# Kernel tuning notes

Hardware: AMD Instinct MI355X
Metric: run time of the kernel (lower is better)

Reference implementation:

```python
import jax, jax.numpy as jnp
import numpy as np

N, E = 50000, 800000
IN, HID, OUT = 128, 128, 64
H, ED = 4, 3
D = HID // H  # per-head dim = 32


def _w(key, shape):
    fan_in = shape[-1]
    return jax.random.normal(key, shape, dtype=jnp.float32) / np.sqrt(fan_in)


def setup_inputs() -> dict:
    key = jax.random.key(0)
    ks = jax.random.split(key, 32)
    inp = {
        "x": jax.random.normal(ks[0], (N, IN), dtype=jnp.float32),
        "edge_index": jax.random.randint(ks[1], (2, E), 0, N, dtype=jnp.int32),
        "edge_attr": jax.random.normal(ks[2], (E, ED), dtype=jnp.float32),
        # layer 1 TransformerConv (bias=False)
        "Wq1": _w(ks[3], (HID, IN)), "Wk1": _w(ks[4], (HID, IN)),
        "Wv1": _w(ks[5], (HID, IN)), "We1": _w(ks[6], (HID, ED)),
        "Ws1": _w(ks[7], (HID, IN)),
        # layer 1 MLP [HID,HID,HID]
        "M1a": _w(ks[8], (HID, HID)), "b1a": jnp.zeros((HID,), jnp.float32),
        "M1b": _w(ks[9], (HID, HID)), "b1b": jnp.zeros((HID,), jnp.float32),
        # layer 2 TransformerConv
        "Wq2": _w(ks[10], (HID, HID)), "Wk2": _w(ks[11], (HID, HID)),
        "Wv2": _w(ks[12], (HID, HID)), "We2": _w(ks[13], (HID, ED)),
        "Ws2": _w(ks[14], (HID, HID)),
        # layer 2 MLP
        "M2a": _w(ks[15], (HID, HID)), "b2a": jnp.zeros((HID,), jnp.float32),
        "M2b": _w(ks[16], (HID, HID)), "b2b": jnp.zeros((HID,), jnp.float32),
        # final MLP [HID,HID,OUT], plain_last=False
        "Wf1": _w(ks[17], (HID, HID)), "bf1": jnp.zeros((HID,), jnp.float32),
        "Wf2": _w(ks[18], (OUT, HID)), "bf2": jnp.zeros((OUT,), jnp.float32),
    }
    return inp


def _gelu(x):
    return jax.nn.gelu(x, approximate=True)


def _transformer_conv(x, src, dst, edge_attr, Wq, Wk, Wv, We, Ws, n_nodes):
    # PyG TransformerConv: x_j = x[src] (message source), x_i = x[dst] (target)
    q = (x @ Wq.T).reshape(n_nodes, H, D)
    e = (edge_attr @ We.T).reshape(-1, H, D)              # [E,H,D]
    k = (x @ Wk.T).reshape(n_nodes, H, D)[src] + e        # [E,H,D]
    v = (x @ Wv.T).reshape(n_nodes, H, D)[src] + e        # [E,H,D]
    alpha = jnp.einsum("ehd,ehd->eh", q[dst], k) / jnp.float32(np.sqrt(D))
    # segment softmax over incoming edges of each target node
    m = jax.ops.segment_max(alpha, dst, num_segments=n_nodes)  # [N,H]
    m = jnp.where(jnp.isfinite(m), m, 0.0)
    p = jnp.exp(alpha - m[dst])
    s = jax.ops.segment_sum(p, dst, num_segments=n_nodes)      # [N,H]
    a = p / jnp.maximum(s[dst], 1e-16)                         # [E,H]
    out = jax.ops.segment_sum(a[:, :, None] * v, dst, num_segments=n_nodes)
    out = out.reshape(n_nodes, H * D)
    # root_weight=True (default): skip connection through lin_skip (no bias)
    return out + x @ Ws.T


def _mlp2(x, Wa, ba, Wb, bb):
    # PyG MLP with plain_last=False: act after every linear, norm=None
    h = _gelu(x @ Wa.T + ba)
    return _gelu(h @ Wb.T + bb)


def reference(x, edge_index, edge_attr,
              Wq1, Wk1, Wv1, We1, Ws1, M1a, b1a, M1b, b1b,
              Wq2, Wk2, Wv2, We2, Ws2, M2a, b2a, M2b, b2b,
              Wf1, bf1, Wf2, bf2):
    n_nodes = x.shape[0]
    src, dst = edge_index[0], edge_index[1]
    h = _transformer_conv(x, src, dst, edge_attr, Wq1, Wk1, Wv1, We1, Ws1, n_nodes)
    h = h + _mlp2(h, M1a, b1a, M1b, b1b)
    h = _transformer_conv(h, src, dst, edge_attr, Wq2, Wk2, Wv2, We2, Ws2, n_nodes)
    h = h + _mlp2(h, M2a, b2a, M2b, b2b)
    return _mlp2(h, Wf1, bf1, Wf2, bf2)
```

## Files before the change

kernel.cpp:

```cpp
#include <hip/hip_runtime.h>
#include <hip/hip_bf16.h>
#include <math.h>

#define NN 50000
#define NE 800000
#define NPAD 50048
#define NB_SCAN 196

typedef unsigned short u16;
typedef unsigned int u32;
typedef __attribute__((ext_vector_type(8))) short short8;
typedef __attribute__((ext_vector_type(4))) float float4v;

__device__ __forceinline__ float us2f(u16 u) { return __uint_as_float(((unsigned)u) << 16); }
__device__ __forceinline__ float blo(u32 u) { return __uint_as_float(u << 16); }
__device__ __forceinline__ float bhi(u32 u) { return __uint_as_float(u & 0xffff0000u); }
__device__ __forceinline__ u16 f2us(float f) {
    unsigned x = __float_as_uint(f);
    return (u16)((x + 0x7FFFu + ((x >> 16) & 1u)) >> 16);
}
__device__ __forceinline__ float gelu_f(float x) {
    float p = x * x;
    float t = x * fmaf(p, 0.0713548162726f, 1.5957691216057308f);
    float e = __expf(-t);
    return x * __builtin_amdgcn_rcpf(1.0f + e);
}
__device__ __forceinline__ void lds_fence() {
    asm volatile("s_waitcnt lgkmcnt(0)" ::: "memory");
}

__device__ __forceinline__ float4v mfma4p(const u16* __restrict__ WP, int tile, int l,
                                          short8 a0, short8 a1, short8 a2, short8 a3) {
    const short8* wp = (const short8*)WP + (size_t)tile * 256 + l;
    short8 b0 = wp[0], b1 = wp[64], b2 = wp[128], b3 = wp[192];
    float4v acc = {0.f, 0.f, 0.f, 0.f};
    acc = __builtin_amdgcn_mfma_f32_16x16x32_bf16(a0, b0, acc, 0, 0, 0);
    acc = __builtin_amdgcn_mfma_f32_16x16x32_bf16(a1, b1, acc, 0, 0, 0);
    acc = __builtin_amdgcn_mfma_f32_16x16x32_bf16(a2, b2, acc, 0, 0, 0);
    acc = __builtin_amdgcn_mfma_f32_16x16x32_bf16(a3, b3, acc, 0, 0, 0);
    return acc;
}


__global__ void k_hist(const int* __restrict__ dstv, int* __restrict__ deg) {
    int e = blockIdx.x * blockDim.x + threadIdx.x;
    if (e < NE) atomicAdd(&deg[dstv[e]], 1);
}

__global__ __launch_bounds__(256) void k_scan1(const int* __restrict__ deg,
                                               int* __restrict__ rowstart,
                                               int* __restrict__ bsum) {
    __shared__ int wtot[4];
    int i = blockIdx.x * 256 + threadIdx.x;
    int lane = threadIdx.x & 63, w = threadIdx.x >> 6;
    int v = (i < NN) ? deg[i] : 0;
    int incl = v;
#pragma unroll
    for (int d = 1; d < 64; d <<= 1) {
        int tv = __shfl_up(incl, d);
        if (lane >= d) incl += tv;
    }
    if (lane == 63) wtot[w] = incl;
    __syncthreads();
    if (threadIdx.x == 0) {
        int s = 0;
#pragma unroll
        for (int j = 0; j < 4; ++j) { int t = wtot[j]; wtot[j] = s; s += t; }
        bsum[blockIdx.x] = s;
    }
    __syncthreads();
    if (i < NN) rowstart[i] = incl - v + wtot[w];
}

__global__ __launch_bounds__(256) void k_scan2(int* __restrict__ bsum) {
    __shared__ int wtot[4];
    int t = threadIdx.x;
    int lane = t & 63, w = t >> 6;
    int v = (t < NB_SCAN) ? bsum[t] : 0;
    int incl = v;
#pragma unroll
    for (int d = 1; d < 64; d <<= 1) {
        int tv = __shfl_up(incl, d);
        if (lane >= d) incl += tv;
    }
    if (lane == 63) wtot[w] = incl;
    __syncthreads();
    if (t == 0) {
        int s = 0;
#pragma unroll
        for (int j = 0; j < 4; ++j) { int tt = wtot[j]; wtot[j] = s; s += tt; }
    }
    __syncthreads();
    if (t < NB_SCAN) bsum[t] = incl - v + wtot[w];
}

__global__ void k_scan3(const int* __restrict__ bsum, int* __restrict__ rowstart,
                        int* __restrict__ cursor) {
    int i = blockIdx.x * 256 + threadIdx.x;
    if (i < NN) {
        int v = rowstart[i] + bsum[blockIdx.x];
        rowstart[i] = v;
        cursor[i] = v;
    }
    if (i == 0) rowstart[NN] = NE;
}

__global__ void k_scatter(const int* __restrict__ srcv, const int* __restrict__ dstv,
                          const float* __restrict__ eattr, int* __restrict__ cursor,
                          int4* __restrict__ rec) {
    int e = blockIdx.x * blockDim.x + threadIdx.x;
    if (e >= NE) return;
    int dst = dstv[e];
    int pos = atomicAdd(&cursor[dst], 1);
    int4 r;
    r.x = srcv[e];
    r.y = __float_as_int(eattr[e * 3 + 0]);
    r.z = __float_as_int(eattr[e * 3 + 1]);
    r.w = __float_as_int(eattr[e * 3 + 2]);
    rec[pos] = r;
}


struct CvtEnt { const float* s; u16* d; int n; };
struct CvtTab { CvtEnt e[14]; };
__global__ void k_cvt_w(CvtTab tab) {
    CvtEnt E = tab.e[blockIdx.x >> 3];
    int chunk = blockIdx.x & 7;
    int per = E.n >> 3;
    int lo = chunk * per, hi = lo + per;
    for (int o = lo + threadIdx.x; o < hi; o += blockDim.x) {
        int tile = o >> 11;
        int q = (o >> 9) & 3;
        int l = (o >> 3) & 63;
        int j = o & 7;
        int row = tile * 16 + (l & 15);
        int col = q * 32 + (l >> 4) * 8 + j;
        E.d[o] = f2us(E.s[row * 128 + col]);
    }
}


__device__ __forceinline__ void stage_plain(u16* buf, int kb, int m, int tt, float4v acc) {
#pragma unroll
    for (int r = 0; r < 4; ++r) buf[(kb * 4 + r) * 136 + tt * 16 + m] = f2us(acc[r]);
}
__device__ __forceinline__ void store128(const u16* buf, u16* dst, int r0w, int coff, int l) {
#pragma unroll
    for (int it = 0; it < 4; ++it) {
        int j = it * 64 + l;
        int row = j >> 4, col = (j & 15) * 8;
        *(uint4*)(dst + (size_t)(r0w + row) * 512 + coff + col) = *(const uint4*)&buf[row * 136 + col];
    }
}
__device__ __forceinline__ void read_frags(const u16* buf, int m, int kb,
                                           short8& f0, short8& f1, short8& f2, short8& f3) {
    const u16* p = buf + m * 136 + kb * 8;
    f0 = *(const short8*)(p);
    f1 = *(const short8*)(p + 32);
    f2 = *(const short8*)(p + 64);
    f3 = *(const short8*)(p + 96);
}



__global__ __launch_bounds__(256, 4) void k_qkvs1(const float* __restrict__ Ain,
                                                  const u16* __restrict__ W,
                                                  u16* __restrict__ QKVS) {
    __shared__ u16 tile[4][16 * 136];
    int tid = threadIdx.x;
    int l = tid & 63, w = tid >> 6, m = l & 15, kb = l >> 4;
    int r0w = blockIdx.x * 64 + w * 16;
    u16* my = tile[w];

    short8 a0, a1, a2, a3;
    {
        const float* ap = Ain + (size_t)(r0w + m) * 128;
        bool ok = (r0w + m) < NN;
        short8* dsts[4] = {&a0, &a1, &a2, &a3};
#pragma unroll
        for (int i = 0; i < 4; ++i) {
            short8 r;
            if (ok) {
                const float* p = ap + (kb + i * 4) * 8;
                float4 f0 = *(const float4*)p;
                float4 f1 = *(const float4*)(p + 4);
                r[0]=(short)f2us(f0.x); r[1]=(short)f2us(f0.y); r[2]=(short)f2us(f0.z); r[3]=(short)f2us(f0.w);
                r[4]=(short)f2us(f1.x); r[5]=(short)f2us(f1.y); r[6]=(short)f2us(f1.z); r[7]=(short)f2us(f1.w);
            } else {
#pragma unroll
                for (int j = 0; j < 8; ++j) r[j] = 0;
            }
            *dsts[i] = r;
        }
    }

    if (blockIdx.y == 0) {
#pragma unroll
        for (int tt = 0; tt < 8; ++tt) stage_plain(my, kb, m, tt, mfma4p(W, tt, l, a0, a1, a2, a3));
        lds_fence();
        store128(my, QKVS, r0w, 0, l);
        lds_fence();
#pragma unroll
        for (int tt = 0; tt < 4; ++tt) {
            float4v acc = mfma4p(W, 8 + tt, l, a0, a1, a2, a3);
            int c = tt * 32 + 8 * (m >> 2) + (m & 3);
#pragma unroll
            for (int r = 0; r < 4; ++r) my[(kb * 4 + r) * 136 + c] = f2us(acc[r]);
        }
#pragma unroll
        for (int tt = 0; tt < 4; ++tt) {
            float4v acc = mfma4p(W, 16 + tt, l, a0, a1, a2, a3);
            int c = tt * 32 + 8 * (m >> 2) + (m & 3) + 4;
#pragma unroll
            for (int r = 0; r < 4; ++r) my[(kb * 4 + r) * 136 + c] = f2us(acc[r]);
        }
        lds_fence();
        store128(my, QKVS, r0w, 128, l);
    } else {
#pragma unroll
        for (int tt = 0; tt < 4; ++tt) {
            float4v acc = mfma4p(W, 12 + tt, l, a0, a1, a2, a3);
            int c = tt * 32 + 8 * (m >> 2) + (m & 3);
#pragma unroll
            for (int r = 0; r < 4; ++r) my[(kb * 4 + r) * 136 + c] = f2us(acc[r]);
        }
#pragma unroll
        for (int tt = 0; tt < 4; ++tt) {
            float4v acc = mfma4p(W, 20 + tt, l, a0, a1, a2, a3);
            int c = tt * 32 + 8 * (m >> 2) + (m & 3) + 4;
#pragma unroll
            for (int r = 0; r < 4; ++r) my[(kb * 4 + r) * 136 + c] = f2us(acc[r]);
        }
        lds_fence();
        store128(my, QKVS, r0w, 256, l);
        lds_fence();
#pragma unroll
        for (int tt = 0; tt < 8; ++tt) stage_plain(my, kb, m, tt, mfma4p(W, 24 + tt, l, a0, a1, a2, a3));
        lds_fence();
        store128(my, QKVS, r0w, 384, l);
    }
}


__global__ __launch_bounds__(256, 4) void k_mlp_qkvs(const u16* __restrict__ Ain,
                                                     const u16* __restrict__ Wm,
                                                     const float* __restrict__ bias1,
                                                     const float* __restrict__ bias2,
                                                     const u16* __restrict__ Wq,
                                                     u16* __restrict__ QKVS) {
    __shared__ u16 shb[4][16 * 136];
    __shared__ u16 t1b[4][16 * 136];
    int tid = threadIdx.x;
    int l = tid & 63, w = tid >> 6, m = l & 15, kb = l >> 4;
    int r0w = blockIdx.x * 64 + w * 16;
    u16* sh = shb[w];
    u16* t1 = t1b[w];

    const short8* arow = (const short8*)(Ain + (size_t)(r0w + m) * 128);
    short8 a0 = arow[kb], a1 = arow[kb + 4], a2 = arow[kb + 8], a3 = arow[kb + 12];
    {
        u16* p = sh + m * 136 + kb * 8;
        *(short8*)(p) = a0;
        *(short8*)(p + 32) = a1;
        *(short8*)(p + 64) = a2;
        *(short8*)(p + 96) = a3;
    }
#pragma unroll
    for (int tt = 0; tt < 8; ++tt) {
        float4v acc = mfma4p(Wm, tt, l, a0, a1, a2, a3);
        float bv = bias1[tt * 16 + m];
#pragma unroll
        for (int r = 0; r < 4; ++r)
            t1[(kb * 4 + r) * 136 + tt * 16 + m] = f2us(gelu_f(acc[r] + bv));
    }
    lds_fence();
    short8 c0, c1, c2, c3;
    read_frags(t1, m, kb, c0, c1, c2, c3);
#pragma unroll
    for (int tt = 0; tt < 8; ++tt) {
        float4v acc = mfma4p(Wm + 16384, tt, l, c0, c1, c2, c3);
        float bv = bias2[tt * 16 + m];
#pragma unroll
        for (int r = 0; r < 4; ++r) {
            int idx = (kb * 4 + r) * 136 + tt * 16 + m;
            sh[idx] = f2us(gelu_f(acc[r] + bv) + us2f(sh[idx]));
        }
    }
    lds_fence();
    short8 h0, h1, h2, h3;
    read_frags(sh, m, kb, h0, h1, h2, h3);

    if (blockIdx.y == 0) {
#pragma unroll
        for (int tt = 0; tt < 8; ++tt) stage_plain(t1, kb, m, tt, mfma4p(Wq, tt, l, h0, h1, h2, h3));
        lds_fence();
        store128(t1, QKVS, r0w, 0, l);
        lds_fence();
#pragma unroll
        for (int tt = 0; tt < 4; ++tt) {
            float4v acc = mfma4p(Wq, 8 + tt, l, h0, h1, h2, h3);
            int c = tt * 32 + 8 * (m >> 2) + (m & 3);
#pragma unroll
            for (int r = 0; r < 4; ++r) t1[(kb * 4 + r) * 136 + c] = f2us(acc[r]);
        }
#pragma unroll
        for (int tt = 0; tt < 4; ++tt) {
            float4v acc = mfma4p(Wq, 16 + tt, l, h0, h1, h2, h3);
            int c = tt * 32 + 8 * (m >> 2) + (m & 3) + 4;
#pragma unroll
            for (int r = 0; r < 4; ++r) t1[(kb * 4 + r) * 136 + c] = f2us(acc[r]);
        }
        lds_fence();
        store128(t1, QKVS, r0w, 128, l);
    } else {
#pragma unroll
        for (int tt = 0; tt < 4; ++tt) {
            float4v acc = mfma4p(Wq, 12 + tt, l, h0, h1, h2, h3);
            int c = tt * 32 + 8 * (m >> 2) + (m & 3);
#pragma unroll
            for (int r = 0; r < 4; ++r) t1[(kb * 4 + r) * 136 + c] = f2us(acc[r]);
        }
#pragma unroll
        for (int tt = 0; tt < 4; ++tt) {
            float4v acc = mfma4p(Wq, 20 + tt, l, h0, h1, h2, h3);
            int c = tt * 32 + 8 * (m >> 2) + (m & 3) + 4;
#pragma unroll
            for (int r = 0; r < 4; ++r) t1[(kb * 4 + r) * 136 + c] = f2us(acc[r]);
        }
        lds_fence();
        store128(t1, QKVS, r0w, 256, l);
        lds_fence();
#pragma unroll
        for (int tt = 0; tt < 8; ++tt) stage_plain(t1, kb, m, tt, mfma4p(Wq, 24 + tt, l, h0, h1, h2, h3));
        lds_fence();
        store128(t1, QKVS, r0w, 384, l);
    }
}


__global__ __launch_bounds__(256, 4) void k_mlp_final(const u16* __restrict__ Ain,
                                                      const u16* __restrict__ Wm,
                                                      const float* __restrict__ bias1,
                                                      const float* __restrict__ bias2,
                                                      const u16* __restrict__ Wf,
                                                      const float* __restrict__ bf1,
                                                      const float* __restrict__ bf2,
                                                      float* __restrict__ outp) {
    __shared__ u16 shb[4][16 * 136];
    __shared__ u16 t1b[4][16 * 136];
    int tid = threadIdx.x;
    int l = tid & 63, w = tid >> 6, m = l & 15, kb = l >> 4;
    int r0w = blockIdx.x * 64 + w * 16;
    u16* sh = shb[w];
    u16* t1 = t1b[w];

    const short8* arow = (const short8*)(Ain + (size_t)(r0w + m) * 128);
    short8 a0 = arow[kb], a1 = arow[kb + 4], a2 = arow[kb + 8], a3 = arow[kb + 12];
    {
        u16* p = sh + m * 136 + kb * 8;
        *(short8*)(p) = a0;
        *(short8*)(p + 32) = a1;
        *(short8*)(p + 64) = a2;
        *(short8*)(p + 96) = a3;
    }
#pragma unroll
    for (int tt = 0; tt < 8; ++tt) {
        float4v acc = mfma4p(Wm, tt, l, a0, a1, a2, a3);
        float bv = bias1[tt * 16 + m];
#pragma unroll
        for (int r = 0; r < 4; ++r)
            t1[(kb * 4 + r) * 136 + tt * 16 + m] = f2us(gelu_f(acc[r] + bv));
    }
    lds_fence();
    short8 c0, c1, c2, c3;
    read_frags(t1, m, kb, c0, c1, c2, c3);
#pragma unroll
    for (int tt = 0; tt < 8; ++tt) {
        float4v acc = mfma4p(Wm + 16384, tt, l, c0, c1, c2, c3);
        float bv = bias2[tt * 16 + m];
#pragma unroll
        for (int r = 0; r < 4; ++r) {
            int idx = (kb * 4 + r) * 136 + tt * 16 + m;
            sh[idx] = f2us(gelu_f(acc[r] + bv) + us2f(sh[idx]));
        }
    }
    lds_fence();
    short8 h0, h1, h2, h3;
    read_frags(sh, m, kb, h0, h1, h2, h3);
#pragma unroll
    for (int tt = 0; tt < 8; ++tt) {
        float4v acc = mfma4p(Wf, tt, l, h0, h1, h2, h3);
        float bv = bf1[tt * 16 + m];
#pragma unroll
        for (int r = 0; r < 4; ++r)
            t1[(kb * 4 + r) * 136 + tt * 16 + m] = f2us(gelu_f(acc[r] + bv));
    }
    lds_fence();
    short8 f0, f1, f2, f3;
    read_frags(t1, m, kb, f0, f1, f2, f3);
    lds_fence();
#pragma unroll
    for (int tt = 0; tt < 4; ++tt) {
        float4v acc = mfma4p(Wf + 16384, tt, l, f0, f1, f2, f3);
        float bv = bf2[tt * 16 + m];
#pragma unroll
        for (int r = 0; r < 4; ++r)
            t1[(kb * 4 + r) * 136 + tt * 16 + m] = f2us(gelu_f(acc[r] + bv));
    }
    lds_fence();
#pragma unroll
    for (int it = 0; it < 2; ++it) {
        int j = it * 64 + l;
        int row = j >> 3, col = (j & 7) * 8;
        int grow = r0w + row;
        if (grow < NN) {
            uint4 pk = *(const uint4*)&t1[row * 136 + col];
            const u16* pv = (const u16*)&pk;
            float* po = outp + (size_t)grow * 64 + col;
            float4 o0 = {us2f(pv[0]), us2f(pv[1]), us2f(pv[2]), us2f(pv[3])};
            float4 o1 = {us2f(pv[4]), us2f(pv[5]), us2f(pv[6]), us2f(pv[7])};
            *(float4*)po = o0;
            *(float4*)(po + 4) = o1;
        }
    }
}


__global__ __launch_bounds__(256) void k_conv(const int* __restrict__ rowstart,
                                              const int4* __restrict__ rec,
                                              const u16* __restrict__ qkvs,
                                              const float* __restrict__ We,
                                              u16* __restrict__ out) {
    int n = blockIdx.x * 4 + (threadIdx.x >> 6);
    int l = threadIdx.x & 63;
    int quarter = l >> 4;
    int li = l & 15;
    int c0 = li * 8;
    const u16* qrow = qkvs + (size_t)n * 512;
    uint4 qu = *(const uint4*)(qrow + c0);
    const float SC = 0.17677669529663687f;
    float q0 = blo(qu.x) * SC, q1 = bhi(qu.x) * SC, q2 = blo(qu.y) * SC, q3 = bhi(qu.y) * SC;
    float q4 = blo(qu.z) * SC, q5 = bhi(qu.z) * SC, q6 = blo(qu.w) * SC, q7 = bhi(qu.w) * SC;
    const float* wep = We + c0 * 3;
    float g0, g1, g2;
    {
        float4 w0 = *(const float4*)(wep);
        float4 w1 = *(const float4*)(wep + 4);
        float4 w2 = *(const float4*)(wep + 8);
        float4 w3 = *(const float4*)(wep + 12);
        float4 w4 = *(const float4*)(wep + 16);
        float4 w5 = *(const float4*)(wep + 20);
        g0 = q0*w0.x + q1*w0.w + q2*w1.z + q3*w2.y + q4*w3.x + q5*w3.w + q6*w4.z + q7*w5.y;
        g1 = q0*w0.y + q1*w1.x + q2*w1.w + q3*w2.z + q4*w3.y + q5*w4.x + q6*w4.w + q7*w5.z;
        g2 = q0*w0.z + q1*w1.y + q2*w2.x + q3*w2.w + q4*w3.z + q5*w4.y + q6*w5.x + q7*w5.w;
    }
    g0 += __shfl_xor(g0, 1); g1 += __shfl_xor(g1, 1); g2 += __shfl_xor(g2, 1);
    g0 += __shfl_xor(g0, 2); g1 += __shfl_xor(g1, 2); g2 += __shfl_xor(g2, 2);

    int e0 = rowstart[n], e1 = rowstart[n + 1];
    int deg = e1 - e0;
    float ss = 0.f, S0 = 0.f, S1 = 0.f, S2 = 0.f;
    float o0 = 0.f, o1 = 0.f, o2 = 0.f, o3 = 0.f, o4 = 0.f, o5 = 0.f, o6 = 0.f, o7 = 0.f;

    if (deg > 0) {
        int iters = (deg + 3) >> 2;
        int eb = e0 + quarter;
        int elast = e1 - 1;
        int4 r0 = rec[min(eb, elast)];
        int4 r1 = rec[min(eb + 4, elast)];
        const u16* kvB = qkvs + 128 + (size_t)li * 16;
        uint4 kA = *(const uint4*)(kvB + (size_t)r0.x * 512);
        uint4 kB = *(const uint4*)(kvB + (size_t)r0.x * 512 + 8);
        for (int i = 0; i < iters; ++i) {
            int4 r2 = rec[min(eb + 4 * (i + 2), elast)];
            const u16* kp = kvB + (size_t)r1.x * 512;
            uint4 nA = *(const uint4*)(kp);
            uint4 nB = *(const uint4*)(kp + 8);
            float part = q0 * blo(kA.x) + q1 * bhi(kA.x) + q2 * blo(kA.y) + q3 * bhi(kA.y)
                       + q4 * blo(kB.x) + q5 * bhi(kB.x) + q6 * blo(kB.y) + q7 * bhi(kB.y);
            part += __shfl_xor(part, 1);
            part += __shfl_xor(part, 2);
            float ea0 = __int_as_float(r0.y), ea1 = __int_as_float(r0.z), ea2 = __int_as_float(r0.w);
            float alpha = fmaf(ea2, g2, fmaf(ea1, g1, fmaf(ea0, g0, part)));
            float p = __expf(fminf(alpha, 80.f));
            p = (eb + 4 * i < e1) ? p : 0.f;
            o0 = fmaf(p, blo(kA.z), o0);
            o1 = fmaf(p, bhi(kA.z), o1);
            o2 = fmaf(p, blo(kA.w), o2);
            o3 = fmaf(p, bhi(kA.w), o3);
            o4 = fmaf(p, blo(kB.z), o4);
            o5 = fmaf(p, bhi(kB.z), o5);
            o6 = fmaf(p, blo(kB.w), o6);
            o7 = fmaf(p, bhi(kB.w), o7);
            ss += p;
            S0 = fmaf(p, ea0, S0);
            S1 = fmaf(p, ea1, S1);
            S2 = fmaf(p, ea2, S2);
            r0 = r1; r1 = r2; kA = nA; kB = nB;
        }
    }
    o0 += __shfl_xor(o0, 16); o1 += __shfl_xor(o1, 16); o2 += __shfl_xor(o2, 16); o3 += __shfl_xor(o3, 16);
    o4 += __shfl_xor(o4, 16); o5 += __shfl_xor(o5, 16); o6 += __shfl_xor(o6, 16); o7 += __shfl_xor(o7, 16);
    ss += __shfl_xor(ss, 16); S0 += __shfl_xor(S0, 16); S1 += __shfl_xor(S1, 16); S2 += __shfl_xor(S2, 16);
    o0 += __shfl_xor(o0, 32); o1 += __shfl_xor(o1, 32); o2 += __shfl_xor(o2, 32); o3 += __shfl_xor(o3, 32);
    o4 += __shfl_xor(o4, 32); o5 += __shfl_xor(o5, 32); o6 += __shfl_xor(o6, 32); o7 += __shfl_xor(o7, 32);
    ss += __shfl_xor(ss, 32); S0 += __shfl_xor(S0, 32); S1 += __shfl_xor(S1, 32); S2 += __shfl_xor(S2, 32);

    float inv = __builtin_amdgcn_rcpf(fmaxf(ss, 1e-16f));
    {
        float4 w0 = *(const float4*)(wep);
        float4 w1 = *(const float4*)(wep + 4);
        float4 w2 = *(const float4*)(wep + 8);
        float4 w3 = *(const float4*)(wep + 12);
        float4 w4 = *(const float4*)(wep + 16);
        float4 w5 = *(const float4*)(wep + 20);
        o0 += w0.x * S0 + w0.y * S1 + w0.z * S2;
        o1 += w0.w * S0 + w1.x * S1 + w1.y * S2;
        o2 += w1.z * S0 + w1.w * S1 + w2.x * S2;
        o3 += w2.y * S0 + w2.z * S1 + w2.w * S2;
        o4 += w3.x * S0 + w3.y * S1 + w3.z * S2;
        o5 += w3.w * S0 + w4.x * S1 + w4.y * S2;
        o6 += w4.z * S0 + w4.w * S1 + w5.x * S2;
        o7 += w5.y * S0 + w5.z * S1 + w5.w * S2;
    }
    uint4 su = *(const uint4*)(qrow + 384 + c0);
    float r0v = fmaf(o0, inv, blo(su.x));
    float r1v = fmaf(o1, inv, bhi(su.x));
    float r2v = fmaf(o2, inv, blo(su.y));
    float r3v = fmaf(o3, inv, bhi(su.y));
    float r4v = fmaf(o4, inv, blo(su.z));
    float r5v = fmaf(o5, inv, bhi(su.z));
    float r6v = fmaf(o6, inv, blo(su.w));
    float r7v = fmaf(o7, inv, bhi(su.w));
    if (quarter == 0) {
        uint4 ou;
        ou.x = (u32)f2us(r0v) | ((u32)f2us(r1v) << 16);
        ou.y = (u32)f2us(r2v) | ((u32)f2us(r3v) << 16);
        ou.z = (u32)f2us(r4v) | ((u32)f2us(r5v) << 16);
        ou.w = (u32)f2us(r6v) | ((u32)f2us(r7v) << 16);
        *(uint4*)(out + (size_t)n * 128 + c0) = ou;
    }
}


extern "C" void kernel_launch(void* const* d_in, const int* in_sizes, int n_in,
                              void* d_out, int out_size, void* d_ws, size_t ws_size,
                              hipStream_t stream) {
    const float* x = (const float*)d_in[0];
    const int* ei = (const int*)d_in[1];
    const float* eattr = (const float*)d_in[2];
    const float* Wq1 = (const float*)d_in[3];
    const float* Wk1 = (const float*)d_in[4];
    const float* Wv1 = (const float*)d_in[5];
    const float* We1 = (const float*)d_in[6];
    const float* Ws1 = (const float*)d_in[7];
    const float* M1a = (const float*)d_in[8];
    const float* b1a = (const float*)d_in[9];
    const float* M1b = (const float*)d_in[10];
    const float* b1b = (const float*)d_in[11];
    const float* Wq2 = (const float*)d_in[12];
    const float* Wk2 = (const float*)d_in[13];
    const float* Wv2 = (const float*)d_in[14];
    const float* We2 = (const float*)d_in[15];
    const float* Ws2 = (const float*)d_in[16];
    const float* M2a = (const float*)d_in[17];
    const float* b2a = (const float*)d_in[18];
    const float* M2b = (const float*)d_in[19];
    const float* b2b = (const float*)d_in[20];
    const float* Wf1 = (const float*)d_in[21];
    const float* bf1 = (const float*)d_in[22];
    const float* Wf2 = (const float*)d_in[23];
    const float* bf2 = (const float*)d_in[24];

    char* ws = (char*)d_ws;
    size_t off = 0;
    auto alloc = [&](size_t bytes) -> void* {
        void* p = ws + off;
        off = (off + bytes + 255) & ~(size_t)255;
        return p;
    };
    int* deg = (int*)alloc((size_t)NN * 4);
    int* rowstart = (int*)alloc((size_t)(NN + 1) * 4);
    int* cursor = (int*)alloc((size_t)NN * 4);
    int* bsum = (int*)alloc((size_t)NB_SCAN * 4);
    int4* rec = (int4*)alloc((size_t)NE * 16);
    u16* QKVS = (u16*)alloc((size_t)NPAD * 512 * 2);
    u16* Ha = (u16*)alloc((size_t)NPAD * 128 * 2);
    u16* WB[14];
    const int wsz[14] = {16384, 16384, 16384, 16384, 16384, 16384, 16384,
                         16384, 16384, 16384, 16384, 16384, 16384, 8192};
    for (int i = 0; i < 14; ++i) WB[i] = (u16*)alloc((size_t)wsz[i] * 2);

    const int* srcv = ei;
    const int* dstv = ei + NE;

    hipMemsetAsync(deg, 0, (size_t)NN * 4, stream);
    k_hist<<<(NE + 255) / 256, 256, 0, stream>>>(dstv, deg);
    k_scan1<<<NB_SCAN, 256, 0, stream>>>(deg, rowstart, bsum);
    k_scan2<<<1, 256, 0, stream>>>(bsum);
    k_scan3<<<NB_SCAN, 256, 0, stream>>>(bsum, rowstart, cursor);
    k_scatter<<<(NE + 255) / 256, 256, 0, stream>>>(srcv, dstv, eattr, cursor, rec);

    CvtTab tab;
    const float* wsrc[14] = {Wq1, Wk1, Wv1, Ws1, Wq2, Wk2, Wv2, Ws2,
                             M1a, M1b, M2a, M2b, Wf1, Wf2};
    for (int i = 0; i < 14; ++i) { tab.e[i].s = wsrc[i]; tab.e[i].d = WB[i]; tab.e[i].n = wsz[i]; }
    k_cvt_w<<<112, 256, 0, stream>>>(tab);

    dim3 blk(256);
    dim3 grd2(NPAD / 64, 2);
    dim3 grd(NPAD / 64);
    dim3 gconv(NN / 4);

    k_qkvs1<<<grd2, blk, 0, stream>>>(x, WB[0], QKVS);
    k_conv<<<gconv, blk, 0, stream>>>(rowstart, rec, QKVS, We1, Ha);
    k_mlp_qkvs<<<grd2, blk, 0, stream>>>(Ha, WB[8], b1a, b1b, WB[4], QKVS);
    k_conv<<<gconv, blk, 0, stream>>>(rowstart, rec, QKVS, We2, Ha);
    k_mlp_final<<<grd, blk, 0, stream>>>(Ha, WB[10], b2a, b2b, WB[12], bf1, bf2, (float*)d_out);
}
```

Measured before the change: 419.7 us.

## Precompute per-node q·We projection in GEMM kernels and shrink GEMM blocks to one wave

The dot product between q and the edge-attribute weights moves out of the per-node conv kernel. It is now computed once per node and head inside the QKVS GEMM kernels and stored in a G buffer. We is repacked into a padded float4 layout so the final edge-attribute correction uses aligned loads, and only the writing quarter of lanes runs it. The GEMM kernels become single-wave 64-thread blocks, and each block computes all 512 output columns instead of splitting across a 2D grid. That change doubles A-fragment reuse but removes the parallel split. It also adds G traffic and more, smaller blocks.

```diff
diff --git a/kernel.cpp b/kernel.cpp
--- a/kernel.cpp
+++ b/kernel.cpp
@@ -139,6 +139,17 @@
     }
 }
 
+__global__ void k_prep_we(const float* __restrict__ We1, const float* __restrict__ We2,
+                          float4* __restrict__ WeP1, float4* __restrict__ WeP2) {
+    int t = threadIdx.x;
+    if (t < 128) {
+        WeP1[t] = make_float4(We1[t * 3], We1[t * 3 + 1], We1[t * 3 + 2], 0.f);
+    } else {
+        int c = t - 128;
+        WeP2[c] = make_float4(We2[c * 3], We2[c * 3 + 1], We2[c * 3 + 2], 0.f);
+    }
+}
+
 
 __device__ __forceinline__ void stage_plain(u16* buf, int kb, int m, int tt, float4v acc) {
 #pragma unroll
@@ -161,16 +172,42 @@
     f3 = *(const short8*)(p + 96);
 }
 
-
-
-__global__ __launch_bounds__(256, 4) void k_qkvs1(const float* __restrict__ Ain,
-                                                  const u16* __restrict__ W,
-                                                  u16* __restrict__ QKVS) {
-    __shared__ u16 tile[4][16 * 136];
-    int tid = threadIdx.x;
-    int l = tid & 63, w = tid >> 6, m = l & 15, kb = l >> 4;
-    int r0w = blockIdx.x * 64 + w * 16;
-    u16* my = tile[w];
+__device__ __forceinline__ void compute_g(const u16* buf, const float4* __restrict__ WeP,
+                                          float4* __restrict__ G, int r0w, int m, int kb) {
+    const u16* qr = buf + m * 136 + kb * 32;
+    short8 qv0 = *(const short8*)(qr);
+    short8 qv1 = *(const short8*)(qr + 8);
+    short8 qv2 = *(const short8*)(qr + 16);
+    short8 qv3 = *(const short8*)(qr + 24);
+    const float4* wp = WeP + kb * 32;
+    float g0 = 0.f, g1 = 0.f, g2 = 0.f;
+    const short8* qs[4] = {&qv0, &qv1, &qv2, &qv3};
+#pragma unroll
+    for (int b = 0; b < 4; ++b) {
+        const u16* qq = (const u16*)qs[b];
+#pragma unroll
+        for (int d = 0; d < 8; ++d) {
+            float qvf = us2f(qq[d]);
+            float4 wv = wp[b * 8 + d];
+            g0 = fmaf(qvf, wv.x, g0);
+            g1 = fmaf(qvf, wv.y, g1);
+            g2 = fmaf(qvf, wv.z, g2);
+        }
+    }
+    G[(size_t)(r0w + m) * 4 + kb] = make_float4(g0, g1, g2, 0.f);
+}
+
+
+
+__global__ __launch_bounds__(64, 4) void k_qkvs1(const float* __restrict__ Ain,
+                                                 const u16* __restrict__ W,
+                                                 const float4* __restrict__ WeP,
+                                                 float4* __restrict__ G,
+                                                 u16* __restrict__ QKVS) {
+    __shared__ u16 my[16 * 136];
+    int l = threadIdx.x;
+    int m = l & 15, kb = l >> 4;
+    int r0w = blockIdx.x * 16;
 
     short8 a0, a1, a2, a3;
     {
@@ -194,67 +231,66 @@
         }
     }
 
-    if (blockIdx.y == 0) {
-#pragma unroll
-        for (int tt = 0; tt < 8; ++tt) stage_plain(my, kb, m, tt, mfma4p(W, tt, l, a0, a1, a2, a3));
-        lds_fence();
-        store128(my, QKVS, r0w, 0, l);
-        lds_fence();
-#pragma unroll
-        for (int tt = 0; tt < 4; ++tt) {
-            float4v acc = mfma4p(W, 8 + tt, l, a0, a1, a2, a3);
-            int c = tt * 32 + 8 * (m >> 2) + (m & 3);
-#pragma unroll
-            for (int r = 0; r < 4; ++r) my[(kb * 4 + r) * 136 + c] = f2us(acc[r]);
-        }
-#pragma unroll
-        for (int tt = 0; tt < 4; ++tt) {
-            float4v acc = mfma4p(W, 16 + tt, l, a0, a1, a2, a3);
-            int c = tt * 32 + 8 * (m >> 2) + (m & 3) + 4;
-#pragma unroll
-            for (int r = 0; r < 4; ++r) my[(kb * 4 + r) * 136 + c] = f2us(acc[r]);
-        }
-        lds_fence();
-        store128(my, QKVS, r0w, 128, l);
-    } else {
-#pragma unroll
-        for (int tt = 0; tt < 4; ++tt) {
-            float4v acc = mfma4p(W, 12 + tt, l, a0, a1, a2, a3);
-            int c = tt * 32 + 8 * (m >> 2) + (m & 3);
-#pragma unroll
-            for (int r = 0; r < 4; ++r) my[(kb * 4 + r) * 136 + c] = f2us(acc[r]);
-        }
-#pragma unroll
-        for (int tt = 0; tt < 4; ++tt) {
-            float4v acc = mfma4p(W, 20 + tt, l, a0, a1, a2, a3);
-            int c = tt * 32 + 8 * (m >> 2) + (m & 3) + 4;
-#pragma unroll
-            for (int r = 0; r < 4; ++r) my[(kb * 4 + r) * 136 + c] = f2us(acc[r]);
-        }
-        lds_fence();
-        store128(my, QKVS, r0w, 256, l);
-        lds_fence();
-#pragma unroll
-        for (int tt = 0; tt < 8; ++tt) stage_plain(my, kb, m, tt, mfma4p(W, 24 + tt, l, a0, a1, a2, a3));
-        lds_fence();
-        store128(my, QKVS, r0w, 384, l);
-    }
-}
-
-
-__global__ __launch_bounds__(256, 4) void k_mlp_qkvs(const u16* __restrict__ Ain,
-                                                     const u16* __restrict__ Wm,
-                                                     const float* __restrict__ bias1,
-                                                     const float* __restrict__ bias2,
-                                                     const u16* __restrict__ Wq,
-                                                     u16* __restrict__ QKVS) {
-    __shared__ u16 shb[4][16 * 136];
-    __shared__ u16 t1b[4][16 * 136];
-    int tid = threadIdx.x;
-    int l = tid & 63, w = tid >> 6, m = l & 15, kb = l >> 4;
-    int r0w = blockIdx.x * 64 + w * 16;
-    u16* sh = shb[w];
-    u16* t1 = t1b[w];
+#pragma unroll
+    for (int tt = 0; tt < 8; ++tt) stage_plain(my, kb, m, tt, mfma4p(W, tt, l, a0, a1, a2, a3));
+    lds_fence();
+    store128(my, QKVS, r0w, 0, l);
+    compute_g(my, WeP, G, r0w, m, kb);
+    lds_fence();
+#pragma unroll
+    for (int tt = 0; tt < 4; ++tt) {
+        float4v acc = mfma4p(W, 8 + tt, l, a0, a1, a2, a3);
+        int c = tt * 32 + 8 * (m >> 2) + (m & 3);
+#pragma unroll
+        for (int r = 0; r < 4; ++r) my[(kb * 4 + r) * 136 + c] = f2us(acc[r]);
+    }
+#pragma unroll
+    for (int tt = 0; tt < 4; ++tt) {
+        float4v acc = mfma4p(W, 16 + tt, l, a0, a1, a2, a3);
+        int c = tt * 32 + 8 * (m >> 2) + (m & 3) + 4;
+#pragma unroll
+        for (int r = 0; r < 4; ++r) my[(kb * 4 + r) * 136 + c] = f2us(acc[r]);
+    }
+    lds_fence();
+    store128(my, QKVS, r0w, 128, l);
+    lds_fence();
+#pragma unroll
+    for (int tt = 0; tt < 4; ++tt) {
+        float4v acc = mfma4p(W, 12 + tt, l, a0, a1, a2, a3);
+        int c = tt * 32 + 8 * (m >> 2) + (m & 3);
+#pragma unroll
+        for (int r = 0; r < 4; ++r) my[(kb * 4 + r) * 136 + c] = f2us(acc[r]);
+    }
+#pragma unroll
+    for (int tt = 0; tt < 4; ++tt) {
+        float4v acc = mfma4p(W, 20 + tt, l, a0, a1, a2, a3);
+        int c = tt * 32 + 8 * (m >> 2) + (m & 3) + 4;
+#pragma unroll
+        for (int r = 0; r < 4; ++r) my[(kb * 4 + r) * 136 + c] = f2us(acc[r]);
+    }
+    lds_fence();
+    store128(my, QKVS, r0w, 256, l);
+    lds_fence();
+#pragma unroll
+    for (int tt = 0; tt < 8; ++tt) stage_plain(my, kb, m, tt, mfma4p(W, 24 + tt, l, a0, a1, a2, a3));
+    lds_fence();
+    store128(my, QKVS, r0w, 384, l);
+}
+
+
+__global__ __launch_bounds__(64, 4) void k_mlp_qkvs(const u16* __restrict__ Ain,
+                                                    const u16* __restrict__ Wm,
+                                                    const float* __restrict__ bias1,
+                                                    const float* __restrict__ bias2,
+                                                    const u16* __restrict__ Wq,
+                                                    const float4* __restrict__ WeP,
+                                                    float4* __restrict__ G,
+                                                    u16* __restrict__ QKVS) {
+    __shared__ u16 sh[16 * 136];
+    __shared__ u16 t1[16 * 136];
+    int l = threadIdx.x;
+    int m = l & 15, kb = l >> 4;
+    int r0w = blockIdx.x * 16;
 
     const short8* arow = (const short8*)(Ain + (size_t)(r0w + m) * 128);
     short8 a0 = arow[kb], a1 = arow[kb + 4], a2 = arow[kb + 8], a3 = arow[kb + 12];
@@ -290,69 +326,66 @@
     short8 h0, h1, h2, h3;
     read_frags(sh, m, kb, h0, h1, h2, h3);
 
-    if (blockIdx.y == 0) {
-#pragma unroll
-        for (int tt = 0; tt < 8; ++tt) stage_plain(t1, kb, m, tt, mfma4p(Wq, tt, l, h0, h1, h2, h3));
-        lds_fence();
-        store128(t1, QKVS, r0w, 0, l);
-        lds_fence();
-#pragma unroll
-        for (int tt = 0; tt < 4; ++tt) {
-            float4v acc = mfma4p(Wq, 8 + tt, l, h0, h1, h2, h3);
-            int c = tt * 32 + 8 * (m >> 2) + (m & 3);
-#pragma unroll
-            for (int r = 0; r < 4; ++r) t1[(kb * 4 + r) * 136 + c] = f2us(acc[r]);
-        }
-#pragma unroll
-        for (int tt = 0; tt < 4; ++tt) {
-            float4v acc = mfma4p(Wq, 16 + tt, l, h0, h1, h2, h3);
-            int c = tt * 32 + 8 * (m >> 2) + (m & 3) + 4;
-#pragma unroll
-            for (int r = 0; r < 4; ++r) t1[(kb * 4 + r) * 136 + c] = f2us(acc[r]);
-        }
-        lds_fence();
-        store128(t1, QKVS, r0w, 128, l);
-    } else {
-#pragma unroll
-        for (int tt = 0; tt < 4; ++tt) {
-            float4v acc = mfma4p(Wq, 12 + tt, l, h0, h1, h2, h3);
-            int c = tt * 32 + 8 * (m >> 2) + (m & 3);
-#pragma unroll
-            for (int r = 0; r < 4; ++r) t1[(kb * 4 + r) * 136 + c] = f2us(acc[r]);
-        }
-#pragma unroll
-        for (int tt = 0; tt < 4; ++tt) {
-            float4v acc = mfma4p(Wq, 20 + tt, l, h0, h1, h2, h3);
-            int c = tt * 32 + 8 * (m >> 2) + (m & 3) + 4;
-#pragma unroll
-            for (int r = 0; r < 4; ++r) t1[(kb * 4 + r) * 136 + c] = f2us(acc[r]);
-        }
-        lds_fence();
-        store128(t1, QKVS, r0w, 256, l);
-        lds_fence();
-#pragma unroll
-        for (int tt = 0; tt < 8; ++tt) stage_plain(t1, kb, m, tt, mfma4p(Wq, 24 + tt, l, h0, h1, h2, h3));
-        lds_fence();
-        store128(t1, QKVS, r0w, 384, l);
-    }
-}
-
-
-__global__ __launch_bounds__(256, 4) void k_mlp_final(const u16* __restrict__ Ain,
-                                                      const u16* __restrict__ Wm,
-                                                      const float* __restrict__ bias1,
-                                                      const float* __restrict__ bias2,
-                                                      const u16* __restrict__ Wf,
-                                                      const float* __restrict__ bf1,
-                                                      const float* __restrict__ bf2,
-                                                      float* __restrict__ outp) {
-    __shared__ u16 shb[4][16 * 136];
-    __shared__ u16 t1b[4][16 * 136];
-    int tid = threadIdx.x;
-    int l = tid & 63, w = tid >> 6, m = l & 15, kb = l >> 4;
-    int r0w = blockIdx.x * 64 + w * 16;
-    u16* sh = shb[w];
-    u16* t1 = t1b[w];
+#pragma unroll
+    for (int tt = 0; tt < 8; ++tt) stage_plain(t1, kb, m, tt, mfma4p(Wq, tt, l, h0, h1, h2, h3));
+    lds_fence();
+    store128(t1, QKVS, r0w, 0, l);
+    compute_g(t1, WeP, G, r0w, m, kb);
+    lds_fence();
+#pragma unroll
+    for (int tt = 0; tt < 4; ++tt) {
+        float4v acc = mfma4p(Wq, 8 + tt, l, h0, h1, h2, h3);
+        int c = tt * 32 + 8 * (m >> 2) + (m & 3);
+#pragma unroll
+        for (int r = 0; r < 4; ++r) t1[(kb * 4 + r) * 136 + c] = f2us(acc[r]);
+    }
+#pragma unroll
+    for (int tt = 0; tt < 4; ++tt) {
+        float4v acc = mfma4p(Wq, 16 + tt, l, h0, h1, h2, h3);
+        int c = tt * 32 + 8 * (m >> 2) + (m & 3) + 4;
+#pragma unroll
+        for (int r = 0; r < 4; ++r) t1[(kb * 4 + r) * 136 + c] = f2us(acc[r]);
+    }
+    lds_fence();
+    store128(t1, QKVS, r0w, 128, l);
+    lds_fence();
+#pragma unroll
+    for (int tt = 0; tt < 4; ++tt) {
+        float4v acc = mfma4p(Wq, 12 + tt, l, h0, h1, h2, h3);
+        int c = tt * 32 + 8 * (m >> 2) + (m & 3);
+#pragma unroll
+        for (int r = 0; r < 4; ++r) t1[(kb * 4 + r) * 136 + c] = f2us(acc[r]);
+    }
+#pragma unroll
+    for (int tt = 0; tt < 4; ++tt) {
+        float4v acc = mfma4p(Wq, 20 + tt, l, h0, h1, h2, h3);
+        int c = tt * 32 + 8 * (m >> 2) + (m & 3) + 4;
+#pragma unroll
+        for (int r = 0; r < 4; ++r) t1[(kb * 4 + r) * 136 + c] = f2us(acc[r]);
+    }
+    lds_fence();
+    store128(t1, QKVS, r0w, 256, l);
+    lds_fence();
+#pragma unroll
+    for (int tt = 0; tt < 8; ++tt) stage_plain(t1, kb, m, tt, mfma4p(Wq, 24 + tt, l, h0, h1, h2, h3));
+    lds_fence();
+    store128(t1, QKVS, r0w, 384, l);
+}
+
+
+__global__ __launch_bounds__(64, 4) void k_mlp_final(const u16* __restrict__ Ain,
+                                                     const u16* __restrict__ Wm,
+                                                     const float* __restrict__ bias1,
+                                                     const float* __restrict__ bias2,
+                                                     const u16* __restrict__ Wf,
+                                                     const float* __restrict__ bf1,
+                                                     const float* __restrict__ bf2,
+                                                     float* __restrict__ outp) {
+    __shared__ u16 sh[16 * 136];
+    __shared__ u16 t1[16 * 136];
+    int l = threadIdx.x;
+    int m = l & 15, kb = l >> 4;
+    int r0w = blockIdx.x * 16;
 
     const short8* arow = (const short8*)(Ain + (size_t)(r0w + m) * 128);
     short8 a0 = arow[kb], a1 = arow[kb + 4], a2 = arow[kb + 8], a3 = arow[kb + 12];
@@ -429,7 +462,8 @@
 __global__ __launch_bounds__(256) void k_conv(const int* __restrict__ rowstart,
                                               const int4* __restrict__ rec,
                                               const u16* __restrict__ qkvs,
-                                              const float* __restrict__ We,
+                                              const float4* __restrict__ WeP,
+                                              const float4* __restrict__ G,
                                               u16* __restrict__ out) {
     int n = blockIdx.x * 4 + (threadIdx.x >> 6);
     int l = threadIdx.x & 63;
@@ -441,21 +475,8 @@
     const float SC = 0.17677669529663687f;
     float q0 = blo(qu.x) * SC, q1 = bhi(qu.x) * SC, q2 = blo(qu.y) * SC, q3 = bhi(qu.y) * SC;
     float q4 = blo(qu.z) * SC, q5 = bhi(qu.z) * SC, q6 = blo(qu.w) * SC, q7 = bhi(qu.w) * SC;
-    const float* wep = We + c0 * 3;
-    float g0, g1, g2;
-    {
-        float4 w0 = *(const float4*)(wep);
-        float4 w1 = *(const float4*)(wep + 4);
-        float4 w2 = *(const float4*)(wep + 8);
-        float4 w3 = *(const float4*)(wep + 12);
-        float4 w4 = *(const float4*)(wep + 16);
-        float4 w5 = *(const float4*)(wep + 20);
-        g0 = q0*w0.x + q1*w0.w + q2*w1.z + q3*w2.y + q4*w3.x + q5*w3.w + q6*w4.z + q7*w5.y;
-        g1 = q0*w0.y + q1*w1.x + q2*w1.w + q3*w2.z + q4*w3.y + q5*w4.x + q6*w4.w + q7*w5.z;
-        g2 = q0*w0.z + q1*w1.y + q2*w2.x + q3*w2.w + q4*w3.z + q5*w4.y + q6*w5.x + q7*w5.w;
-    }
-    g0 += __shfl_xor(g0, 1); g1 += __shfl_xor(g1, 1); g2 += __shfl_xor(g2, 1);
-    g0 += __shfl_xor(g0, 2); g1 += __shfl_xor(g1, 2); g2 += __shfl_xor(g2, 2);
+    float4 gg = G[(size_t)n * 4 + (li >> 2)];
+    float g0 = gg.x * SC, g1 = gg.y * SC, g2 = gg.z * SC;
 
     int e0 = rowstart[n], e1 = rowstart[n + 1];
     int deg = e1 - e0;
@@ -506,33 +527,27 @@
     o4 += __shfl_xor(o4, 32); o5 += __shfl_xor(o5, 32); o6 += __shfl_xor(o6, 32); o7 += __shfl_xor(o7, 32);
     ss += __shfl_xor(ss, 32); S0 += __shfl_xor(S0, 32); S1 += __shfl_xor(S1, 32); S2 += __shfl_xor(S2, 32);
 
-    float inv = __builtin_amdgcn_rcpf(fmaxf(ss, 1e-16f));
-    {
-        float4 w0 = *(const float4*)(wep);
-        float4 w1 = *(const float4*)(wep + 4);
-        float4 w2 = *(const float4*)(wep + 8);
-        float4 w3 = *(const float4*)(wep + 12);
-        float4 w4 = *(const float4*)(wep + 16);
-        float4 w5 = *(const float4*)(wep + 20);
+    if (quarter == 0) {
+        float inv = __builtin_amdgcn_rcpf(fmaxf(ss, 1e-16f));
+        float4 w0 = WeP[c0 + 0], w1 = WeP[c0 + 1], w2 = WeP[c0 + 2], w3 = WeP[c0 + 3];
+        float4 w4 = WeP[c0 + 4], w5 = WeP[c0 + 5], w6 = WeP[c0 + 6], w7 = WeP[c0 + 7];
         o0 += w0.x * S0 + w0.y * S1 + w0.z * S2;
-        o1 += w0.w * S0 + w1.x * S1 + w1.y * S2;
-        o2 += w1.z * S0 + w1.w * S1 + w2.x * S2;
-        o3 += w2.y * S0 + w2.z * S1 + w2.w * S2;
-        o4 += w3.x * S0 + w3.y * S1 + w3.z * S2;
-        o5 += w3.w * S0 + w4.x * S1 + w4.y * S2;
-        o6 += w4.z * S0 + w4.w * S1 + w5.x * S2;
-        o7 += w5.y * S0 + w5.z * S1 + w5.w * S2;
-    }
-    uint4 su = *(const uint4*)(qrow + 384 + c0);
-    float r0v = fmaf(o0, inv, blo(su.x));
-    float r1v = fmaf(o1, inv, bhi(su.x));
-    float r2v = fmaf(o2, inv, blo(su.y));
-    float r3v = fmaf(o3, inv, bhi(su.y));
-    float r4v = fmaf(o4, inv, blo(su.z));
-    float r5v = fmaf(o5, inv, bhi(su.z));
-    float r6v = fmaf(o6, inv, blo(su.w));
-    float r7v = fmaf(o7, inv, bhi(su.w));
-    if (quarter == 0) {
+        o1 += w1.x * S0 + w1.y * S1 + w1.z * S2;
+        o2 += w2.x * S0 + w2.y * S1 + w2.z * S2;
+        o3 += w3.x * S0 + w3.y * S1 + w3.z * S2;
+        o4 += w4.x * S0 + w4.y * S1 + w4.z * S2;
+        o5 += w5.x * S0 + w5.y * S1 + w5.z * S2;
+        o6 += w6.x * S0 + w6.y * S1 + w6.z * S2;
+        o7 += w7.x * S0 + w7.y * S1 + w7.z * S2;
+        uint4 su = *(const uint4*)(qrow + 384 + c0);
+        float r0v = fmaf(o0, inv, blo(su.x));
+        float r1v = fmaf(o1, inv, bhi(su.x));
+        float r2v = fmaf(o2, inv, blo(su.y));
+        float r3v = fmaf(o3, inv, bhi(su.y));
+        float r4v = fmaf(o4, inv, blo(su.z));
+        float r5v = fmaf(o5, inv, bhi(su.z));
+        float r6v = fmaf(o6, inv, blo(su.w));
+        float r7v = fmaf(o7, inv, bhi(su.w));
         uint4 ou;
         ou.x = (u32)f2us(r0v) | ((u32)f2us(r1v) << 16);
         ou.y = (u32)f2us(r2v) | ((u32)f2us(r3v) << 16);
@@ -586,6 +601,9 @@
     int4* rec = (int4*)alloc((size_t)NE * 16);
     u16* QKVS = (u16*)alloc((size_t)NPAD * 512 * 2);
     u16* Ha = (u16*)alloc((size_t)NPAD * 128 * 2);
+    float4* G = (float4*)alloc((size_t)NPAD * 4 * 16);
+    float4* WeP1 = (float4*)alloc(128 * 16);
+    float4* WeP2 = (float4*)alloc(128 * 16);
     u16* WB[14];
     const int wsz[14] = {16384, 16384, 16384, 16384, 16384, 16384, 16384,
                          16384, 16384, 16384, 16384, 16384, 16384, 8192};
@@ -606,15 +624,14 @@
                              M1a, M1b, M2a, M2b, Wf1, Wf2};
     for (int i = 0; i < 14; ++i) { tab.e[i].s = wsrc[i]; tab.e[i].d = WB[i]; tab.e[i].n = wsz[i]; }
     k_cvt_w<<<112, 256, 0, stream>>>(tab);
-
-    dim3 blk(256);
-    dim3 grd2(NPAD / 64, 2);
-    dim3 grd(NPAD / 64);
+    k_prep_we<<<1, 256, 0, stream>>>(We1, We2, WeP1, WeP2);
+
+    dim3 gg(NPAD / 16);
     dim3 gconv(NN / 4);
 
-    k_qkvs1<<<grd2, blk, 0, stream>>>(x, WB[0], QKVS);
-    k_conv<<<gconv, blk, 0, stream>>>(rowstart, rec, QKVS, We1, Ha);
-    k_mlp_qkvs<<<grd2, blk, 0, stream>>>(Ha, WB[8], b1a, b1b, WB[4], QKVS);
-    k_conv<<<gconv, blk, 0, stream>>>(rowstart, rec, QKVS, We2, Ha);
-    k_mlp_final<<<grd, blk, 0, stream>>>(Ha, WB[10], b2a, b2b, WB[12], bf1, bf2, (float*)d_out);
-}
+    k_qkvs1<<<gg, 64, 0, stream>>>(x, WB[0], WeP1, G, QKVS);
+    k_conv<<<gconv, 256, 0, stream>>>(rowstart, rec, QKVS, WeP1, G, Ha);
+    k_mlp_qkvs<<<gg, 64, 0, stream>>>(Ha, WB[8], b1a, b1b, WB[4], WeP2, G, QKVS);
+    k_conv<<<gconv, 256, 0, stream>>>(rowstart, rec, QKVS, WeP2, G, Ha);
+    k_mlp_final<<<gg, 64, 0, stream>>>(Ha, WB[10], b2a, b2b, WB[12], bf1, bf2, (float*)d_out);
+}
```

Result: no change. 412.1 us (-1.8%).
